# Performance work log

Measured on AMD Instinct MI355X. Metric: run time of the kernel, lower is better.

The kernel has to match this reference:

```python
import jax, jax.numpy as jnp
import numpy as np

N = 4096      # nodes
F = 128       # input feature dim
HEADS = 8     # attention_num
U = 8         # units per head


def setup_inputs() -> dict:
    key = jax.random.key(0)
    k_a, k_h, k_w, k_al, k_ar = jax.random.split(key, 5)
    A = jax.random.randint(k_a, (N, N), 0, 2).astype(jnp.float32)   # dense 0/1 adjacency
    H = jax.random.normal(k_h, (N, F), dtype=jnp.float32)
    W = jax.random.normal(k_w, (HEADS, F, U), dtype=jnp.float32) * 0.1
    a_left = jax.random.normal(k_al, (HEADS, U), dtype=jnp.float32) * 0.1
    a_right = jax.random.normal(k_ar, (HEADS, U), dtype=jnp.float32) * 0.1
    return {"A": A, "H": H, "W": W, "a_left": a_left, "a_right": a_right}


def reference(A, H, W, a_left, a_right):
    # Per-head attention logits: E[h,i,j] = e_left[h,i] + e_right[h,j]
    e_l = jnp.einsum('nf,hfu,hu->hn', H, W, a_left)    # [HEADS, N]
    e_r = jnp.einsum('nf,hfu,hu->hn', H, W, a_right)   # [HEADS, N]
    E = e_l[:, :, None] + e_r[:, None, :]              # [HEADS, N, N]
    # Faithful to original: denominator uses exp(E * A) (zeros in A -> exp(0)=1)
    denom = jnp.sum(jnp.exp(E * A[None]), axis=-1, keepdims=True)   # [HEADS, N, 1]
    Alpha = jnp.exp(E) / denom * A[None]               # masked attention weights
    # Aggregate then project: elu(Alpha @ H @ W) per head
    out = jax.nn.elu(jnp.einsum('hij,jf,hfu->hiu', Alpha, H, W))    # [HEADS, N, U]
    # is_output_layer=False -> concat heads along feature dim: [N, HEADS*U]
    return jnp.transpose(out, (1, 0, 2)).reshape(H.shape[0], HEADS * U)
```

## Files before the change

kernel.cpp:

```cpp
#include <hip/hip_runtime.h>
#include <hip/hip_bf16.h>

#define NN 4096
#define FF 128
#define NC 80
#define HPAD 136
#define LSTR 84

typedef __attribute__((ext_vector_type(4))) float float4v;
typedef __attribute__((ext_vector_type(4))) unsigned int uint4v;
typedef __attribute__((ext_vector_type(8))) short short8;
typedef __attribute__((ext_vector_type(8))) unsigned short ushort8;
typedef __attribute__((ext_vector_type(4))) unsigned short ushort4v;

static __device__ inline unsigned short bfb(float x) {
    __hip_bfloat16 b = __float2bfloat16(x);
    return *(unsigned short*)&b;
}
static __device__ inline float bff(unsigned short u) {
    __hip_bfloat16 b = *(__hip_bfloat16*)&u;
    return __bfloat162float(b);
}

__global__ __launch_bounds__(128) void gat_prep(const float* __restrict__ H,
                                                const float* __restrict__ W,
                                                const float* __restrict__ al,
                                                const float* __restrict__ ar,
                                                float* __restrict__ expEl,
                                                __hip_bfloat16* __restrict__ Bp)
{
    __shared__ unsigned short Hhi[32 * HPAD], Hlo[32 * HPAD];
    __shared__ unsigned short Whi[16 * NC * 8], Wlo[16 * NC * 8];
    const int t  = threadIdx.x;
    const int j0 = blockIdx.x * 32;

    {
        const int jr = t >> 2, f0 = (t & 3) * 32;
        const float* src = H + (size_t)(j0 + jr) * FF + f0;
        unsigned short* dh = Hhi + jr * HPAD + f0;
        unsigned short* dl = Hlo + jr * HPAD + f0;
        #pragma unroll
        for (int i = 0; i < 32; i += 4) {
            float4v x = *(const float4v*)(src + i);
            ushort4v hv, lv;
            #pragma unroll
            for (int c2 = 0; c2 < 4; ++c2) {
                unsigned short h = bfb(x[c2]);
                hv[c2] = h;
                lv[c2] = bfb(x[c2] - bff(h));
            }
            *(ushort4v*)(dh + i) = hv;
            *(ushort4v*)(dl + i) = lv;
        }
    }
    {
        const int hu = t & 63;
        const int fb = (t >> 6) * 64;
        const float* wsrc = W + (size_t)(hu >> 3) * (FF * 8) + (hu & 7);
        #pragma unroll
        for (int g8 = 0; g8 < 8; ++g8) {
            const int f0 = fb + g8 * 8;
            ushort8 hv, lv;
            #pragma unroll
            for (int i = 0; i < 8; ++i) {
                float x = wsrc[(size_t)(f0 + i) * 8];
                unsigned short h = bfb(x);
                hv[i] = h; lv[i] = bfb(x - bff(h));
            }
            const int g = (f0 >> 5) * 4 + ((f0 >> 3) & 3);
            *(ushort8*)&Whi[((size_t)g * NC + hu) * 8] = hv;
            *(ushort8*)&Wlo[((size_t)g * NC + hu) * 8] = lv;
        }
    }
    {
        const int h  = t >> 4;
        const int f0 = (t & 15) * 8;
        float arv[8], alv[8];
        #pragma unroll
        for (int u = 0; u < 8; ++u) { arv[u] = ar[h * 8 + u]; alv[u] = al[h * 8 + u]; }
        ushort8 rh, rl, lh, ll;
        #pragma unroll
        for (int i = 0; i < 8; ++i) {
            const float* wp = W + (size_t)h * (FF * 8) + (size_t)(f0 + i) * 8;
            float sr = 0.f, sl = 0.f;
            #pragma unroll
            for (int u = 0; u < 8; ++u) { float w = wp[u]; sr += w * arv[u]; sl += w * alv[u]; }
            unsigned short a = bfb(sr); rh[i] = a; rl[i] = bfb(sr - bff(a));
            unsigned short b = bfb(sl); lh[i] = b; ll[i] = bfb(sl - bff(b));
        }
        const int g = (f0 >> 5) * 4 + ((f0 >> 3) & 3);
        *(ushort8*)&Whi[((size_t)g * NC + 64 + h) * 8] = rh;
        *(ushort8*)&Wlo[((size_t)g * NC + 64 + h) * 8] = rl;
        *(ushort8*)&Whi[((size_t)g * NC + 72 + h) * 8] = lh;
        *(ushort8*)&Wlo[((size_t)g * NC + 72 + h) * 8] = ll;
    }
    __syncthreads();

    const int w = t >> 6, lane = t & 63;
    const int m16 = lane & 15, q = lane >> 4;

    float4v acc[5] = {};
    #pragma unroll
    for (int kt = 0; kt < 4; ++kt) {
        short8 ahi = *(const short8*)&Hhi[(w * 16 + m16) * HPAD + kt * 32 + q * 8];
        short8 alo = *(const short8*)&Hlo[(w * 16 + m16) * HPAD + kt * 32 + q * 8];
        #pragma unroll
        for (int nt = 0; nt < 5; ++nt) {
            short8 bhi = *(const short8*)&Whi[((size_t)(kt * 4 + q) * NC + nt * 16 + m16) * 8];
            short8 blo = *(const short8*)&Wlo[((size_t)(kt * 4 + q) * NC + nt * 16 + m16) * 8];
            acc[nt] = __builtin_amdgcn_mfma_f32_16x16x32_bf16(ahi, bhi, acc[nt], 0, 0, 0);
            acc[nt] = __builtin_amdgcn_mfma_f32_16x16x32_bf16(alo, bhi, acc[nt], 0, 0, 0);
            acc[nt] = __builtin_amdgcn_mfma_f32_16x16x32_bf16(ahi, blo, acc[nt], 0, 0, 0);
        }
    }

    const int jbase = j0 + w * 16 + q * 4;
    float ex[4];
    #pragma unroll
    for (int r = 0; r < 4; ++r) ex[r] = expf(acc[4][r]);
    if (m16 >= 8) {
        #pragma unroll
        for (int r = 0; r < 4; ++r)
            expEl[(m16 - 8) * NN + jbase + r] = ex[r];
    }
    #pragma unroll
    for (int r = 0; r < 4; ++r) {
        const int j = jbase + r;
        const size_t base = ((size_t)((j >> 5) * 4 + ((j >> 3) & 3)) * NC) * 8 + (j & 7);
        #pragma unroll
        for (int nt = 0; nt < 4; ++nt) {
            const int srcl = (lane & 48) | (nt * 2 + (m16 >> 3));
            const float er = __shfl(ex[r], srcl);
            Bp[base + (size_t)(nt * 16 + m16) * 8] = __float2bfloat16(er * acc[nt][r]);
        }
        const float v = (m16 < 8) ? ex[r] : (m16 == 8 ? 1.0f : 0.0f);
        Bp[base + (size_t)(64 + m16) * 8] = __float2bfloat16(v);
    }
}

__global__ __launch_bounds__(512) void gat_gemm(const float* __restrict__ A,
                                                const __hip_bfloat16* __restrict__ Bp,
                                                const float* __restrict__ expEl,
                                                float* __restrict__ out)
{
    __shared__ float Ls[8 * 16 * LSTR];
    const int rb   = blockIdx.x;
    const int wave = threadIdx.x >> 6;
    const int lane = threadIdx.x & 63;
    const int m16  = lane & 15;
    const int q    = lane >> 4;
    const int row0 = rb * 16;

    float4v acc[5] = {};

    const int k0 = wave * 512;
    const unsigned int* Au = (const unsigned int*)A;
    const short* Bs = (const short*)Bp;
    const unsigned int* arow = Au + (size_t)(row0 + m16) * NN + q * 8;

    uint4v a0 = *(const uint4v*)(arow + k0);
    uint4v a1 = *(const uint4v*)(arow + k0 + 4);

    #pragma unroll 4
    for (int kt = 0; kt < 16; ++kt) {
        const int kk = k0 + kt * 32;
        short8 afrag;
        afrag[0] = (short)(a0[0] >> 16); afrag[1] = (short)(a0[1] >> 16);
        afrag[2] = (short)(a0[2] >> 16); afrag[3] = (short)(a0[3] >> 16);
        afrag[4] = (short)(a1[0] >> 16); afrag[5] = (short)(a1[1] >> 16);
        afrag[6] = (short)(a1[2] >> 16); afrag[7] = (short)(a1[3] >> 16);

        if (kt + 1 < 16) {
            a0 = *(const uint4v*)(arow + kk + 32);
            a1 = *(const uint4v*)(arow + kk + 36);
        }

        const int ktg = kk >> 5;
        const short8* bbase = (const short8*)(Bs + ((size_t)(ktg * 4 + q) * NC) * 8);
        #pragma unroll
        for (int nt = 0; nt < 5; ++nt) {
            short8 bfrag = bbase[nt * 16 + m16];
            acc[nt] = __builtin_amdgcn_mfma_f32_16x16x32_bf16(afrag, bfrag, acc[nt], 0, 0, 0);
        }
    }

    float* Lw = Ls + wave * (16 * LSTR);
    #pragma unroll
    for (int nt = 0; nt < 5; ++nt) {
        #pragma unroll
        for (int r = 0; r < 4; ++r)
            Lw[(q * 4 + r) * LSTR + nt * 16 + m16] = acc[nt][r];
    }
    __syncthreads();

    #pragma unroll
    for (int p = threadIdx.x; p < 1024; p += 512) {
        const int il = p >> 6;
        const int c  = p & 63;
        const int h  = c >> 3;
        float T = 0.f, S = 0.f, dg = 0.f;
        #pragma unroll
        for (int w = 0; w < 8; ++w) {
            const float* rowp = Ls + w * (16 * LSTR) + il * LSTR;
            T  += rowp[c];
            S  += rowp[64 + h];
            dg += rowp[72];
        }
        const float el = expEl[h * NN + row0 + il];
        const float denom = ((float)NN - dg) + el * S;
        const float x = el * T / denom;
        out[(size_t)(row0 + il) * 64 + c] = x > 0.f ? x : expf(x) - 1.f;
    }
}

extern "C" void kernel_launch(void* const* d_in, const int* in_sizes, int n_in,
                              void* d_out, int out_size, void* d_ws, size_t ws_size,
                              hipStream_t stream) {
    const float* A  = (const float*)d_in[0];
    const float* H  = (const float*)d_in[1];
    const float* W  = (const float*)d_in[2];
    const float* al = (const float*)d_in[3];
    const float* ar = (const float*)d_in[4];
    float* out = (float*)d_out;

    float* expEl = (float*)d_ws;
    __hip_bfloat16* Bp = (__hip_bfloat16*)((char*)d_ws + 131072);

    gat_prep<<<NN / 32, 128, 0, stream>>>(H, W, al, ar, expEl, Bp);
    gat_gemm<<<NN / 16, 512, 0, stream>>>(A, Bp, expEl, out);
}
```

Baseline: 116.4 us.

## Split W preprocessing into its own kernel, widen GEMM split-K, add nontemporal A loads

```diff
diff --git a/kernel.cpp b/kernel.cpp
--- a/kernel.cpp
+++ b/kernel.cpp
@@ -4,14 +4,11 @@
 #define NN 4096
 #define FF 128
 #define NC 80
-#define HPAD 136
 #define LSTR 84
 
 typedef __attribute__((ext_vector_type(4))) float float4v;
 typedef __attribute__((ext_vector_type(4))) unsigned int uint4v;
 typedef __attribute__((ext_vector_type(8))) short short8;
-typedef __attribute__((ext_vector_type(8))) unsigned short ushort8;
-typedef __attribute__((ext_vector_type(4))) unsigned short ushort4v;
 
 static __device__ inline unsigned short bfb(float x) {
     __hip_bfloat16 b = __float2bfloat16(x);
@@ -21,100 +18,88 @@
     __hip_bfloat16 b = *(__hip_bfloat16*)&u;
     return __bfloat162float(b);
 }
-
-__global__ __launch_bounds__(128) void gat_prep(const float* __restrict__ H,
-                                                const float* __restrict__ W,
-                                                const float* __restrict__ al,
-                                                const float* __restrict__ ar,
-                                                float* __restrict__ expEl,
-                                                __hip_bfloat16* __restrict__ Bp)
+static __device__ inline uint4v ntload(const unsigned int* p) {
+    return __builtin_nontemporal_load((const uint4v*)p);
+}
+
+__global__ __launch_bounds__(640) void gat_wsplit(const float* __restrict__ W,
+                                                  const float* __restrict__ al,
+                                                  const float* __restrict__ ar,
+                                                  __hip_bfloat16* __restrict__ Wphi,
+                                                  __hip_bfloat16* __restrict__ Wplo)
 {
-    __shared__ unsigned short Hhi[32 * HPAD], Hlo[32 * HPAD];
-    __shared__ unsigned short Whi[16 * NC * 8], Wlo[16 * NC * 8];
-    const int t  = threadIdx.x;
-    const int j0 = blockIdx.x * 32;
-
-    {
-        const int jr = t >> 2, f0 = (t & 3) * 32;
-        const float* src = H + (size_t)(j0 + jr) * FF + f0;
-        unsigned short* dh = Hhi + jr * HPAD + f0;
-        unsigned short* dl = Hlo + jr * HPAD + f0;
-        #pragma unroll
-        for (int i = 0; i < 32; i += 4) {
-            float4v x = *(const float4v*)(src + i);
-            ushort4v hv, lv;
+    const int c  = threadIdx.x;
+    const int f0 = threadIdx.y * 16;
+    float av[8];
+    const int hc = (c - 64) & 7;
+    if (c >= 64) {
+        const float* ap = (c < 72) ? ar : al;
+        #pragma unroll
+        for (int u = 0; u < 8; ++u) av[u] = ap[hc * 8 + u];
+    }
+    #pragma unroll
+    for (int i = 0; i < 16; ++i) {
+        const int f = f0 + i;
+        float val;
+        if (c < 64) {
+            val = W[(size_t)(c >> 3) * (FF * 8) + (size_t)f * 8 + (c & 7)];
+        } else {
+            const float* wp = W + (size_t)hc * (FF * 8) + (size_t)f * 8;
+            float s = 0.f;
             #pragma unroll
-            for (int c2 = 0; c2 < 4; ++c2) {
-                unsigned short h = bfb(x[c2]);
-                hv[c2] = h;
-                lv[c2] = bfb(x[c2] - bff(h));
-            }
-            *(ushort4v*)(dh + i) = hv;
-            *(ushort4v*)(dl + i) = lv;
-        }
-    }
-    {
-        const int hu = t & 63;
-        const int fb = (t >> 6) * 64;
-        const float* wsrc = W + (size_t)(hu >> 3) * (FF * 8) + (hu & 7);
-        #pragma unroll
-        for (int g8 = 0; g8 < 8; ++g8) {
-            const int f0 = fb + g8 * 8;
-            ushort8 hv, lv;
-            #pragma unroll
-            for (int i = 0; i < 8; ++i) {
-                float x = wsrc[(size_t)(f0 + i) * 8];
-                unsigned short h = bfb(x);
-                hv[i] = h; lv[i] = bfb(x - bff(h));
-            }
-            const int g = (f0 >> 5) * 4 + ((f0 >> 3) & 3);
-            *(ushort8*)&Whi[((size_t)g * NC + hu) * 8] = hv;
-            *(ushort8*)&Wlo[((size_t)g * NC + hu) * 8] = lv;
-        }
-    }
-    {
-        const int h  = t >> 4;
-        const int f0 = (t & 15) * 8;
-        float arv[8], alv[8];
-        #pragma unroll
-        for (int u = 0; u < 8; ++u) { arv[u] = ar[h * 8 + u]; alv[u] = al[h * 8 + u]; }
-        ushort8 rh, rl, lh, ll;
-        #pragma unroll
-        for (int i = 0; i < 8; ++i) {
-            const float* wp = W + (size_t)h * (FF * 8) + (size_t)(f0 + i) * 8;
-            float sr = 0.f, sl = 0.f;
-            #pragma unroll
-            for (int u = 0; u < 8; ++u) { float w = wp[u]; sr += w * arv[u]; sl += w * alv[u]; }
-            unsigned short a = bfb(sr); rh[i] = a; rl[i] = bfb(sr - bff(a));
-            unsigned short b = bfb(sl); lh[i] = b; ll[i] = bfb(sl - bff(b));
-        }
-        const int g = (f0 >> 5) * 4 + ((f0 >> 3) & 3);
-        *(ushort8*)&Whi[((size_t)g * NC + 64 + h) * 8] = rh;
-        *(ushort8*)&Wlo[((size_t)g * NC + 64 + h) * 8] = rl;
-        *(ushort8*)&Whi[((size_t)g * NC + 72 + h) * 8] = lh;
-        *(ushort8*)&Wlo[((size_t)g * NC + 72 + h) * 8] = ll;
-    }
-    __syncthreads();
-
-    const int w = t >> 6, lane = t & 63;
+            for (int u = 0; u < 8; ++u) s += wp[u] * av[u];
+            val = s;
+        }
+        const unsigned short h = bfb(val);
+        const unsigned short l = bfb(val - bff(h));
+        const int g = (f >> 5) * 4 + ((f >> 3) & 3);
+        const size_t idx = ((size_t)g * NC + c) * 8 + (f & 7);
+        Wphi[idx] = *(const __hip_bfloat16*)&h;
+        Wplo[idx] = *(const __hip_bfloat16*)&l;
+    }
+}
+
+__global__ __launch_bounds__(64) void gat_prep(const float* __restrict__ H,
+                                               const __hip_bfloat16* __restrict__ Wphi,
+                                               const __hip_bfloat16* __restrict__ Wplo,
+                                               float* __restrict__ expEl,
+                                               __hip_bfloat16* __restrict__ Bp)
+{
+    const int lane = threadIdx.x;
+    const int j0 = blockIdx.x * 16;
     const int m16 = lane & 15, q = lane >> 4;
+    const short* Whs = (const short*)Wphi;
+    const short* Wls = (const short*)Wplo;
 
     float4v acc[5] = {};
     #pragma unroll
     for (int kt = 0; kt < 4; ++kt) {
-        short8 ahi = *(const short8*)&Hhi[(w * 16 + m16) * HPAD + kt * 32 + q * 8];
-        short8 alo = *(const short8*)&Hlo[(w * 16 + m16) * HPAD + kt * 32 + q * 8];
+        const float* hp = H + (size_t)(j0 + m16) * FF + kt * 32 + q * 8;
+        float4v x0 = *(const float4v*)hp;
+        float4v x1 = *(const float4v*)(hp + 4);
+        short8 ahi, alo;
+        #pragma unroll
+        for (int i = 0; i < 4; ++i) {
+            const unsigned short h0 = bfb(x0[i]);
+            ahi[i] = (short)h0;
+            alo[i] = (short)bfb(x0[i] - bff(h0));
+            const unsigned short h1 = bfb(x1[i]);
+            ahi[4 + i] = (short)h1;
+            alo[4 + i] = (short)bfb(x1[i] - bff(h1));
+        }
+        const short8* bh = (const short8*)(Whs + (size_t)(kt * 4 + q) * NC * 8);
+        const short8* bl = (const short8*)(Wls + (size_t)(kt * 4 + q) * NC * 8);
         #pragma unroll
         for (int nt = 0; nt < 5; ++nt) {
-            short8 bhi = *(const short8*)&Whi[((size_t)(kt * 4 + q) * NC + nt * 16 + m16) * 8];
-            short8 blo = *(const short8*)&Wlo[((size_t)(kt * 4 + q) * NC + nt * 16 + m16) * 8];
+            short8 bhi = bh[nt * 16 + m16];
+            short8 blo = bl[nt * 16 + m16];
             acc[nt] = __builtin_amdgcn_mfma_f32_16x16x32_bf16(ahi, bhi, acc[nt], 0, 0, 0);
             acc[nt] = __builtin_amdgcn_mfma_f32_16x16x32_bf16(alo, bhi, acc[nt], 0, 0, 0);
             acc[nt] = __builtin_amdgcn_mfma_f32_16x16x32_bf16(ahi, blo, acc[nt], 0, 0, 0);
         }
     }
 
-    const int jbase = j0 + w * 16 + q * 4;
+    const int jbase = j0 + q * 4;
     float ex[4];
     #pragma unroll
     for (int r = 0; r < 4; ++r) ex[r] = expf(acc[4][r]);
@@ -138,12 +123,12 @@
     }
 }
 
-__global__ __launch_bounds__(512) void gat_gemm(const float* __restrict__ A,
-                                                const __hip_bfloat16* __restrict__ Bp,
-                                                const float* __restrict__ expEl,
-                                                float* __restrict__ out)
+__global__ __launch_bounds__(1024) void gat_gemm(const float* __restrict__ A,
+                                                 const __hip_bfloat16* __restrict__ Bp,
+                                                 const float* __restrict__ expEl,
+                                                 float* __restrict__ out)
 {
-    __shared__ float Ls[8 * 16 * LSTR];
+    __shared__ float Ls[16 * 16 * LSTR];
     const int rb   = blockIdx.x;
     const int wave = threadIdx.x >> 6;
     const int lane = threadIdx.x & 63;
@@ -153,29 +138,30 @@
 
     float4v acc[5] = {};
 
-    const int k0 = wave * 512;
+    const int k0 = wave * 256;
     const unsigned int* Au = (const unsigned int*)A;
     const short* Bs = (const short*)Bp;
-    const unsigned int* arow = Au + (size_t)(row0 + m16) * NN + q * 8;
-
-    uint4v a0 = *(const uint4v*)(arow + k0);
-    uint4v a1 = *(const uint4v*)(arow + k0 + 4);
-
-    #pragma unroll 4
-    for (int kt = 0; kt < 16; ++kt) {
-        const int kk = k0 + kt * 32;
+    const unsigned int* arow = Au + (size_t)(row0 + m16) * NN + q * 8 + k0;
+
+    uint4v a0[2], a1[2];
+    a0[0] = ntload(arow);      a1[0] = ntload(arow + 4);
+    a0[1] = ntload(arow + 32); a1[1] = ntload(arow + 36);
+
+    #pragma unroll
+    for (int kt = 0; kt < 8; ++kt) {
+        const int cur = kt & 1;
         short8 afrag;
-        afrag[0] = (short)(a0[0] >> 16); afrag[1] = (short)(a0[1] >> 16);
-        afrag[2] = (short)(a0[2] >> 16); afrag[3] = (short)(a0[3] >> 16);
-        afrag[4] = (short)(a1[0] >> 16); afrag[5] = (short)(a1[1] >> 16);
-        afrag[6] = (short)(a1[2] >> 16); afrag[7] = (short)(a1[3] >> 16);
-
-        if (kt + 1 < 16) {
-            a0 = *(const uint4v*)(arow + kk + 32);
-            a1 = *(const uint4v*)(arow + kk + 36);
-        }
-
-        const int ktg = kk >> 5;
+        afrag[0] = (short)(a0[cur][0] >> 16); afrag[1] = (short)(a0[cur][1] >> 16);
+        afrag[2] = (short)(a0[cur][2] >> 16); afrag[3] = (short)(a0[cur][3] >> 16);
+        afrag[4] = (short)(a1[cur][0] >> 16); afrag[5] = (short)(a1[cur][1] >> 16);
+        afrag[6] = (short)(a1[cur][2] >> 16); afrag[7] = (short)(a1[cur][3] >> 16);
+
+        if (kt + 2 < 8) {
+            a0[cur] = ntload(arow + (kt + 2) * 32);
+            a1[cur] = ntload(arow + (kt + 2) * 32 + 4);
+        }
+
+        const int ktg = wave * 8 + kt;
         const short8* bbase = (const short8*)(Bs + ((size_t)(ktg * 4 + q) * NC) * 8);
         #pragma unroll
         for (int nt = 0; nt < 5; ++nt) {
@@ -193,14 +179,14 @@
     }
     __syncthreads();
 
-    #pragma unroll
-    for (int p = threadIdx.x; p < 1024; p += 512) {
+    {
+        const int p  = threadIdx.x;
         const int il = p >> 6;
         const int c  = p & 63;
         const int h  = c >> 3;
         float T = 0.f, S = 0.f, dg = 0.f;
         #pragma unroll
-        for (int w = 0; w < 8; ++w) {
+        for (int w = 0; w < 16; ++w) {
             const float* rowp = Ls + w * (16 * LSTR) + il * LSTR;
             T  += rowp[c];
             S  += rowp[64 + h];
@@ -224,8 +210,11 @@
     float* out = (float*)d_out;
 
     float* expEl = (float*)d_ws;
-    __hip_bfloat16* Bp = (__hip_bfloat16*)((char*)d_ws + 131072);
-
-    gat_prep<<<NN / 32, 128, 0, stream>>>(H, W, al, ar, expEl, Bp);
-    gat_gemm<<<NN / 16, 512, 0, stream>>>(A, Bp, expEl, out);
-}
+    __hip_bfloat16* Bp   = (__hip_bfloat16*)((char*)d_ws + 131072);
+    __hip_bfloat16* Wphi = (__hip_bfloat16*)((char*)d_ws + 131072 + 655360);
+    __hip_bfloat16* Wplo = (__hip_bfloat16*)((char*)d_ws + 131072 + 655360 + 20480);
+
+    gat_wsplit<<<1, dim3(80, 8), 0, stream>>>(W, al, ar, Wphi, Wplo);
+    gat_prep<<<NN / 16, 64, 0, stream>>>(H, Wphi, Wplo, expEl, Bp);
+    gat_gemm<<<NN / 16, 1024, 0, stream>>>(A, Bp, expEl, out);
+}
```

After: 132.9 us. 1.14x slower.
